# Optimization experiments

Hardware: AMD Instinct MI355X
Metric: run time of the kernel (lower is better)

Reference implementation:

```python
import jax, jax.numpy as jnp
import numpy as np

D_MODEL, N_HEADS, D_FF = 1024, 16, 4096
D_K = D_MODEL // N_HEADS
EPS = 1e-5


def setup_inputs() -> dict:
    key = jax.random.key(0)
    ks = jax.random.split(key, 16)
    s = 0.02
    p = {
        'x': jax.random.normal(ks[0], (2, 2048, D_MODEL), jnp.float32),
        'Wq': jax.random.normal(ks[1], (D_MODEL, D_MODEL), jnp.float32) * s,
        'bq': jnp.zeros((D_MODEL,), jnp.float32),
        'Wk': jax.random.normal(ks[2], (D_MODEL, D_MODEL), jnp.float32) * s,
        'bk': jnp.zeros((D_MODEL,), jnp.float32),
        'Wv': jax.random.normal(ks[3], (D_MODEL, D_MODEL), jnp.float32) * s,
        'bv': jnp.zeros((D_MODEL,), jnp.float32),
        'Wo': jax.random.normal(ks[4], (D_MODEL, D_MODEL), jnp.float32) * s,
        'bo': jnp.zeros((D_MODEL,), jnp.float32),
        'g1': jnp.ones((D_MODEL,), jnp.float32),
        'b1': jnp.zeros((D_MODEL,), jnp.float32),
        'W1': jax.random.normal(ks[5], (D_MODEL, D_FF), jnp.float32) * s,
        'bf1': jnp.zeros((D_FF,), jnp.float32),
        'W2': jax.random.normal(ks[6], (D_FF, D_MODEL), jnp.float32) * s,
        'bf2': jnp.zeros((D_MODEL,), jnp.float32),
        'g2': jnp.ones((D_MODEL,), jnp.float32),
        'b2': jnp.zeros((D_MODEL,), jnp.float32),
    }
    return p


def _layernorm(x, g, b):
    mu = jnp.mean(x, axis=-1, keepdims=True)
    var = jnp.var(x, axis=-1, keepdims=True)
    return (x - mu) * jax.lax.rsqrt(var + EPS) * g + b


def reference(x, Wq, bq, Wk, bk, Wv, bv, Wo, bo, g1, b1, W1, bf1, W2, bf2, g2, b2):
    B, S, _ = x.shape
    # project and split heads -> [B, H, S, d_k]
    def heads(y):
        return y.reshape(B, S, N_HEADS, D_K).transpose(0, 2, 1, 3)
    Q = heads(x @ Wq + bq)
    K = heads(x @ Wk + bk)
    V = heads(x @ Wv + bv)
    scores = jnp.einsum('bhqd,bhkd->bhqk', Q, K) / np.sqrt(D_K).astype(np.float32)
    attn = jax.nn.softmax(scores, axis=-1)  # dropout = identity (eval)
    ctx = jnp.einsum('bhqk,bhkd->bhqd', attn, V)
    ctx = ctx.transpose(0, 2, 1, 3).reshape(B, S, D_MODEL)
    attn_out = ctx @ Wo + bo
    h = _layernorm(x + attn_out, g1, b1)
    ff = (jax.nn.gelu(h @ W1 + bf1, approximate=False)) @ W2 + bf2
    out = _layernorm(h + ff, g2, b2)
    return out, attn
```

## Files before the change

kernel.cpp:

```cpp
#include <hip/hip_runtime.h>
#include <stdint.h>

#define SEQ 2048
#define BATCH 2
#define NH 16
#define DKH 64
#define DM 1024
#define DFF 4096
#define MTOT (BATCH*SEQ)

typedef __attribute__((ext_vector_type(8))) short bf16x8;
typedef __attribute__((ext_vector_type(4))) float f32x4;
typedef unsigned short ushort_t;

__device__ __forceinline__ unsigned short f2bf(float f) {
  union { float f; unsigned u; } c; c.f = f;
  return (unsigned short)((c.u + 0x7fffu + ((c.u >> 16) & 1u)) >> 16);
}

__device__ __forceinline__ void gload_lds16(const void* g, void* l) {
  __builtin_amdgcn_global_load_lds((__attribute__((address_space(1))) unsigned int*)g,
                                   (__attribute__((address_space(3))) unsigned int*)l,
                                   16, 0, 0);
}


__global__ __launch_bounds__(256) void conv_bf16(const float* __restrict__ X,
                                                 unsigned short* __restrict__ O, int n) {
  const int i = blockIdx.x * 256 + threadIdx.x;
  const int idx = i * 4;
  if (idx >= n) return;
  const float4 f = *(const float4*)(X + idx);
  ushort4 u; u.x = f2bf(f.x); u.y = f2bf(f.y); u.z = f2bf(f.z); u.w = f2bf(f.w);
  *(ushort4*)(O + idx) = u;
}

__global__ __launch_bounds__(256) void trans_conv(const float* __restrict__ W,
                                                  unsigned short* __restrict__ Wt,
                                                  int K, int N) {
  __shared__ float t[32][33];
  const int n0 = blockIdx.x * 32, k0 = blockIdx.y * 32;
  const int tx = threadIdx.x & 31, ty = threadIdx.x >> 5;
#pragma unroll
  for (int i = 0; i < 4; ++i)
    t[ty + i * 8][tx] = W[(long)(k0 + ty + i * 8) * N + n0 + tx];
  __syncthreads();
#pragma unroll
  for (int i = 0; i < 4; ++i)
    Wt[(long)(n0 + ty + i * 8) * K + k0 + tx] = f2bf(t[tx][ty + i * 8]);
}

__global__ __launch_bounds__(256) void trans_v(const unsigned short* __restrict__ V,
                                               unsigned short* __restrict__ Vt) {
  __shared__ unsigned short t[32][33];
  const int z = blockIdx.z, b = z >> 4, h = z & 15;
  const int s0 = blockIdx.x * 32, d0 = blockIdx.y * 32;
  const int tx = threadIdx.x & 31, ty = threadIdx.x >> 5;
#pragma unroll
  for (int i = 0; i < 4; ++i)
    t[ty + i * 8][tx] = V[(long)(b * SEQ + s0 + ty + i * 8) * DM + h * DKH + d0 + tx];
  __syncthreads();
#pragma unroll
  for (int i = 0; i < 4; ++i)
    Vt[((long)z * DKH + d0 + ty + i * 8) * SEQ + s0 + tx] = t[tx][ty + i * 8];
}

template <int EPI>
__global__ __launch_bounds__(256) void gemm_bt(
    const unsigned short* __restrict__ A, const unsigned short* __restrict__ Bt,
    float* __restrict__ Cf, unsigned short* __restrict__ Cbf,
    const float* __restrict__ bias, const float* __restrict__ resid,
    int M, int N, int K, int lda, int ldb, int ldc) {
  __shared__ unsigned short ldsA[128 * 32];
  __shared__ unsigned short ldsB[128 * 32];

  const int tid = threadIdx.x;
  const int lane = tid & 63, wave = tid >> 6;
  const int quad = lane >> 4, l16 = lane & 15;
  const int wm = (wave >> 1) * 64, wn = (wave & 1) * 64;
  const long tileM = (long)blockIdx.x * 128;
  const long tileN = (long)blockIdx.y * 128;

  const int srow = tid >> 2;
  const int scol = (tid & 3) * 8;
  const unsigned short* aSrc = A + (tileM + srow) * lda + scol;
  const unsigned short* bSrc = Bt + (tileN + srow) * ldb + scol;
  unsigned short* aDst = &ldsA[tid * 8];
  unsigned short* bDst = &ldsB[tid * 8];
  const long aRow64 = 64L * lda, bRow64 = 64L * ldb;

  f32x4 acc[4][4];
#pragma unroll
  for (int i = 0; i < 4; ++i)
#pragma unroll
    for (int j = 0; j < 4; ++j)
#pragma unroll
      for (int r = 0; r < 4; ++r) acc[i][j][r] = 0.f;

  for (int k0 = 0; k0 < K; k0 += 32) {
    __syncthreads();
    gload_lds16(aSrc + k0, aDst);
    gload_lds16(aSrc + aRow64 + k0, aDst + 2048);
    gload_lds16(bSrc + k0, bDst);
    gload_lds16(bSrc + bRow64 + k0, bDst + 2048);
    __syncthreads();

    bf16x8 aF[4], bF[4];
#pragma unroll
    for (int i = 0; i < 4; ++i)
      aF[i] = *(const bf16x8*)&ldsA[(wm + i * 16 + l16) * 32 + quad * 8];
#pragma unroll
    for (int j = 0; j < 4; ++j)
      bF[j] = *(const bf16x8*)&ldsB[(wn + j * 16 + l16) * 32 + quad * 8];
#pragma unroll
    for (int i = 0; i < 4; ++i)
#pragma unroll
      for (int j = 0; j < 4; ++j)
        acc[i][j] = __builtin_amdgcn_mfma_f32_16x16x32_bf16(aF[i], bF[j], acc[i][j], 0, 0, 0);
  }

#pragma unroll
  for (int i = 0; i < 4; ++i) {
    const long mb = tileM + wm + i * 16 + quad * 4;
#pragma unroll
    for (int j = 0; j < 4; ++j) {
      const long n = tileN + wn + j * 16 + l16;
      const float bv = bias[n];
#pragma unroll
      for (int r = 0; r < 4; ++r) {
        const long m = mb + r;
        const long idx = m * ldc + n;
        const float v = acc[i][j][r];
        if (EPI == 0) {
          Cbf[idx] = f2bf(v + bv);
        } else if (EPI == 2) {
          Cf[idx] = v + bv + resid[idx];
        } else {
          const float tt = v + bv;
          Cbf[idx] = f2bf(0.5f * tt * (1.f + erff(tt * 0.70710678118654752f)));
        }
      }
    }
  }
}

__global__ __launch_bounds__(256) void attn_stats(const unsigned short* __restrict__ Qbf,
                                                  const unsigned short* __restrict__ Kbf,
                                                  float2* __restrict__ stats) {
  const int z = blockIdx.z, b = z >> 4, h = z & 15;
  const int m0 = blockIdx.x * 128;

  __shared__ unsigned short ldsQ[2 * 128 * 32];
  __shared__ unsigned short ldsK[2 * 128 * 32];
  __shared__ float2 sm[4][64];

  const int tid = threadIdx.x;
  const int lane = tid & 63, wave = tid >> 6;
  const int quad = lane >> 4, l16 = lane & 15;
  const int wm = (wave >> 1) * 64, wn = (wave & 1) * 64;

  const unsigned short* Qbase = Qbf + ((long)(b * SEQ + m0)) * DM + h * DKH;
#pragma unroll
  for (int it = 0; it < 4; ++it) {
    const int c = it * 256 + tid;
    const int slab = c >> 9, row = (c >> 2) & 127, q = c & 3;
    gload_lds16(Qbase + (long)row * DM + slab * 32 + q * 8, &ldsQ[c * 8]);
  }

  float rm[4][4], rl[4][4];
#pragma unroll
  for (int i = 0; i < 4; ++i)
#pragma unroll
    for (int r = 0; r < 4; ++r) { rm[i][r] = -1e30f; rl[i][r] = 0.f; }

  for (int n = 0; n < 16; ++n) {
    __syncthreads();
    const unsigned short* Kbase = Kbf + ((long)(b * SEQ + n * 128)) * DM + h * DKH;
#pragma unroll
    for (int it = 0; it < 4; ++it) {
      const int c = it * 256 + tid;
      const int slab = c >> 9, row = (c >> 2) & 127, q = c & 3;
      gload_lds16(Kbase + (long)row * DM + slab * 32 + q * 8, &ldsK[c * 8]);
    }
    __syncthreads();

    f32x4 acc[4][4];
#pragma unroll
    for (int i = 0; i < 4; ++i)
#pragma unroll
      for (int j = 0; j < 4; ++j)
#pragma unroll
        for (int r = 0; r < 4; ++r) acc[i][j][r] = 0.f;

#pragma unroll
    for (int s = 0; s < 2; ++s) {
      bf16x8 aF[4], bF[4];
#pragma unroll
      for (int i = 0; i < 4; ++i)
        aF[i] = *(const bf16x8*)&ldsQ[(s * 128 + wm + i * 16 + l16) * 32 + quad * 8];
#pragma unroll
      for (int j = 0; j < 4; ++j)
        bF[j] = *(const bf16x8*)&ldsK[(s * 128 + wn + j * 16 + l16) * 32 + quad * 8];
#pragma unroll
      for (int i = 0; i < 4; ++i)
#pragma unroll
        for (int j = 0; j < 4; ++j)
          acc[i][j] = __builtin_amdgcn_mfma_f32_16x16x32_bf16(aF[i], bF[j], acc[i][j], 0, 0, 0);
    }

#pragma unroll
    for (int i = 0; i < 4; ++i)
#pragma unroll
      for (int r = 0; r < 4; ++r) {
        float v0 = acc[i][0][r] * 0.125f, v1 = acc[i][1][r] * 0.125f;
        float v2 = acc[i][2][r] * 0.125f, v3 = acc[i][3][r] * 0.125f;
        float tm = fmaxf(fmaxf(v0, v1), fmaxf(v2, v3));
#pragma unroll
        for (int o = 1; o < 16; o <<= 1) tm = fmaxf(tm, __shfl_xor(tm, o));
        const float mnew = fmaxf(rm[i][r], tm);
        float s4 = __expf(v0 - mnew) + __expf(v1 - mnew) +
                   __expf(v2 - mnew) + __expf(v3 - mnew);
#pragma unroll
        for (int o = 1; o < 16; o <<= 1) s4 += __shfl_xor(s4, o);
        rl[i][r] = rl[i][r] * __expf(rm[i][r] - mnew) + s4;
        rm[i][r] = mnew;
      }
  }

  if (l16 == 0) {
#pragma unroll
    for (int i = 0; i < 4; ++i)
#pragma unroll
      for (int r = 0; r < 4; ++r)
        sm[wave][i * 16 + quad * 4 + r] = make_float2(rm[i][r], rl[i][r]);
  }
  __syncthreads();
  if (tid < 128) {
    const int row = tid, g = row >> 6;
    const float2 a = sm[g * 2 + 0][row & 63];
    const float2 bb = sm[g * 2 + 1][row & 63];
    const float M = fmaxf(a.x, bb.x);
    const float Z = a.y * __expf(a.x - M) + bb.y * __expf(bb.x - M);
    stats[(long)z * SEQ + m0 + row] = make_float2(M, 1.f / Z);
  }
}

__global__ __launch_bounds__(256) void attn_fused(const unsigned short* __restrict__ Qbf,
                                                  const unsigned short* __restrict__ Kbf,
                                                  const unsigned short* __restrict__ Vt,
                                                  const float2* __restrict__ stats,
                                                  float* __restrict__ attn,
                                                  unsigned short* __restrict__ Ctx) {
  const int z = blockIdx.z, b = z >> 4, h = z & 15;
  const int m0 = blockIdx.x * 128;

  __shared__ unsigned short ldsQ[2 * 128 * 32];
  __shared__ unsigned short ldsK[2 * 128 * 32];
  __shared__ unsigned short ldsV[4 * 64 * 32];
  __shared__ unsigned short ldsP[4 * 128 * 32];

  const int tid = threadIdx.x;
  const int lane = tid & 63, wave = tid >> 6;
  const int quad = lane >> 4, l16 = lane & 15;
  const int wm = (wave >> 1) * 64, wn = (wave & 1) * 64;
  const int wm2 = (wave >> 1) * 64, wn2 = (wave & 1) * 32;

  const unsigned short* Qbase = Qbf + ((long)(b * SEQ + m0)) * DM + h * DKH;
#pragma unroll
  for (int it = 0; it < 4; ++it) {
    const int c = it * 256 + tid;
    const int slab = c >> 9, row = (c >> 2) & 127, q = c & 3;
    gload_lds16(Qbase + (long)row * DM + slab * 32 + q * 8, &ldsQ[c * 8]);
  }

  float sM[4][4], sI[4][4];
#pragma unroll
  for (int i = 0; i < 4; ++i)
#pragma unroll
    for (int r = 0; r < 4; ++r) {
      const float2 st = stats[(long)z * SEQ + m0 + wm + i * 16 + quad * 4 + r];
      sM[i][r] = st.x; sI[i][r] = st.y;
    }

  f32x4 acc_o[4][2];
#pragma unroll
  for (int i = 0; i < 4; ++i)
#pragma unroll
    for (int j = 0; j < 2; ++j)
#pragma unroll
      for (int r = 0; r < 4; ++r) acc_o[i][j][r] = 0.f;

  for (int n = 0; n < 16; ++n) {
    __syncthreads();
    const unsigned short* Kbase = Kbf + ((long)(b * SEQ + n * 128)) * DM + h * DKH;
#pragma unroll
    for (int it = 0; it < 4; ++it) {
      const int c = it * 256 + tid;
      const int slab = c >> 9, row = (c >> 2) & 127, q = c & 3;
      gload_lds16(Kbase + (long)row * DM + slab * 32 + q * 8, &ldsK[c * 8]);
    }
    const unsigned short* Vbase = Vt + (long)z * DKH * SEQ + n * 128;
#pragma unroll
    for (int it = 0; it < 4; ++it) {
      const int c = it * 256 + tid;
      const int slab = c >> 8, row = (c >> 2) & 63, q = c & 3;
      gload_lds16(Vbase + (long)row * SEQ + slab * 32 + q * 8, &ldsV[c * 8]);
    }
    __syncthreads();

    f32x4 acc[4][4];
#pragma unroll
    for (int i = 0; i < 4; ++i)
#pragma unroll
      for (int j = 0; j < 4; ++j)
#pragma unroll
        for (int r = 0; r < 4; ++r) acc[i][j][r] = 0.f;
#pragma unroll
    for (int s = 0; s < 2; ++s) {
      bf16x8 aF[4], bF[4];
#pragma unroll
      for (int i = 0; i < 4; ++i)
        aF[i] = *(const bf16x8*)&ldsQ[(s * 128 + wm + i * 16 + l16) * 32 + quad * 8];
#pragma unroll
      for (int j = 0; j < 4; ++j)
        bF[j] = *(const bf16x8*)&ldsK[(s * 128 + wn + j * 16 + l16) * 32 + quad * 8];
#pragma unroll
      for (int i = 0; i < 4; ++i)
#pragma unroll
        for (int j = 0; j < 4; ++j)
          acc[i][j] = __builtin_amdgcn_mfma_f32_16x16x32_bf16(aF[i], bF[j], acc[i][j], 0, 0, 0);
    }

    float* attnBase = attn + (long)z * SEQ * SEQ + (long)m0 * SEQ + n * 128;
#pragma unroll
    for (int i = 0; i < 4; ++i)
#pragma unroll
      for (int r = 0; r < 4; ++r) {
        const int rowl = wm + i * 16 + quad * 4 + r;
        const float M = sM[i][r], I = sI[i][r];
#pragma unroll
        for (int j = 0; j < 4; ++j) {
          const int col = wn + j * 16 + l16;
          const float p = __expf(acc[i][j][r] * 0.125f - M) * I;
          attnBase[(long)rowl * SEQ + col] = p;
          ldsP[((col >> 5) * 128 + rowl) * 32 + (col & 31)] = f2bf(p);
        }
      }
    __syncthreads();

#pragma unroll
    for (int slab = 0; slab < 4; ++slab) {
      bf16x8 aF[4], bF[2];
#pragma unroll
      for (int i = 0; i < 4; ++i)
        aF[i] = *(const bf16x8*)&ldsP[(slab * 128 + wm2 + i * 16 + l16) * 32 + quad * 8];
#pragma unroll
      for (int j = 0; j < 2; ++j)
        bF[j] = *(const bf16x8*)&ldsV[(slab * 64 + wn2 + j * 16 + l16) * 32 + quad * 8];
#pragma unroll
      for (int i = 0; i < 4; ++i)
#pragma unroll
        for (int j = 0; j < 2; ++j)
          acc_o[i][j] = __builtin_amdgcn_mfma_f32_16x16x32_bf16(aF[i], bF[j], acc_o[i][j], 0, 0, 0);
    }
  }

#pragma unroll
  for (int i = 0; i < 4; ++i)
#pragma unroll
    for (int j = 0; j < 2; ++j) {
      const int d = h * DKH + wn2 + j * 16 + l16;
#pragma unroll
      for (int r = 0; r < 4; ++r) {
        const long m = (long)b * SEQ + m0 + wm2 + i * 16 + quad * 4 + r;
        Ctx[m * DM + d] = f2bf(acc_o[i][j][r]);
      }
    }
}

__global__ __launch_bounds__(256) void layernorm_row(const float* __restrict__ Y,
                                                     const float* __restrict__ g,
                                                     const float* __restrict__ bb,
                                                     float* __restrict__ outF,
                                                     unsigned short* __restrict__ outBf) {
  const long row = blockIdx.x;
  const float* p = Y + row * DM;
  const int tid = threadIdx.x;
  const float4 v = *(const float4*)(p + tid * 4);
  float s = v.x + v.y + v.z + v.w;
  float ss = v.x * v.x + v.y * v.y + v.z * v.z + v.w * v.w;
#pragma unroll
  for (int o = 32; o > 0; o >>= 1) { s += __shfl_xor(s, o); ss += __shfl_xor(ss, o); }
  __shared__ float rs[4], rss[4];
  if ((tid & 63) == 0) { rs[tid >> 6] = s; rss[tid >> 6] = ss; }
  __syncthreads();
  s = rs[0] + rs[1] + rs[2] + rs[3];
  ss = rss[0] + rss[1] + rss[2] + rss[3];
  const float mu = s * (1.f / DM);
  const float var = ss * (1.f / DM) - mu * mu;
  const float rstd = rsqrtf(var + 1e-5f);
  const float4 gv = *(const float4*)(g + tid * 4);
  const float4 bv = *(const float4*)(bb + tid * 4);
  float4 o;
  o.x = (v.x - mu) * rstd * gv.x + bv.x;
  o.y = (v.y - mu) * rstd * gv.y + bv.y;
  o.z = (v.z - mu) * rstd * gv.z + bv.z;
  o.w = (v.w - mu) * rstd * gv.w + bv.w;
  *(float4*)(outF + row * DM + tid * 4) = o;
  if (outBf) {
    ushort4 u; u.x = f2bf(o.x); u.y = f2bf(o.y); u.z = f2bf(o.z); u.w = f2bf(o.w);
    *(ushort4*)(outBf + row * DM + tid * 4) = u;
  }
}

extern "C" void kernel_launch(void* const* d_in, const int* in_sizes, int n_in,
                              void* d_out, int out_size, void* d_ws, size_t ws_size,
                              hipStream_t stream) {
  (void)in_sizes; (void)n_in; (void)out_size; (void)ws_size;
  const float* x  = (const float*)d_in[0];
  const float* Wq = (const float*)d_in[1];
  const float* bq = (const float*)d_in[2];
  const float* Wk = (const float*)d_in[3];
  const float* bk = (const float*)d_in[4];
  const float* Wv = (const float*)d_in[5];
  const float* bv = (const float*)d_in[6];
  const float* Wo = (const float*)d_in[7];
  const float* bo = (const float*)d_in[8];
  const float* g1 = (const float*)d_in[9];
  const float* b1 = (const float*)d_in[10];
  const float* W1 = (const float*)d_in[11];
  const float* bf1 = (const float*)d_in[12];
  const float* W2 = (const float*)d_in[13];
  const float* bf2 = (const float*)d_in[14];
  const float* g2 = (const float*)d_in[15];
  const float* b2 = (const float*)d_in[16];

  float* out  = (float*)d_out;
  float* attn = out + (long)MTOT * DM;

  char* w = (char*)d_ws;
  const long MB = 1024L * 1024L;
  unsigned short* Wqt = (unsigned short*)(w + 0 * MB);
  unsigned short* Wkt = (unsigned short*)(w + 2 * MB);
  unsigned short* Wvt = (unsigned short*)(w + 4 * MB);
  unsigned short* Wot = (unsigned short*)(w + 6 * MB);
  unsigned short* W1t = (unsigned short*)(w + 8 * MB);
  unsigned short* W2t = (unsigned short*)(w + 16 * MB);
  unsigned short* xbf = (unsigned short*)(w + 24 * MB);
  unsigned short* hbf = xbf;
  unsigned short* Qbf = (unsigned short*)(w + 32 * MB);
  unsigned short* Kbf = (unsigned short*)(w + 40 * MB);
  unsigned short* Vt  = (unsigned short*)(w + 48 * MB);
  unsigned short* Vbf = (unsigned short*)(w + 56 * MB);
  unsigned short* ctxbf = Vbf;
  unsigned short* ffbf  = Qbf;
  float* y = (float*)(w + 64 * MB);
  float2* stats = (float2*)(w + 64 * MB);
  float* h = (float*)(w + 80 * MB);

  const dim3 blk(256);

  conv_bf16<<<dim3(MTOT * DM / 1024), blk, 0, stream>>>(x, xbf, MTOT * DM);
  trans_conv<<<dim3(DM / 32, DM / 32), blk, 0, stream>>>(Wq, Wqt, DM, DM);
  trans_conv<<<dim3(DM / 32, DM / 32), blk, 0, stream>>>(Wk, Wkt, DM, DM);
  trans_conv<<<dim3(DM / 32, DM / 32), blk, 0, stream>>>(Wv, Wvt, DM, DM);
  trans_conv<<<dim3(DM / 32, DM / 32), blk, 0, stream>>>(Wo, Wot, DM, DM);
  trans_conv<<<dim3(DFF / 32, DM / 32), blk, 0, stream>>>(W1, W1t, DM, DFF);
  trans_conv<<<dim3(DM / 32, DFF / 32), blk, 0, stream>>>(W2, W2t, DFF, DM);

  gemm_bt<0><<<dim3(MTOT / 128, DM / 128), blk, 0, stream>>>(
      xbf, Wqt, nullptr, Qbf, bq, nullptr, MTOT, DM, DM, DM, DM, DM);
  gemm_bt<0><<<dim3(MTOT / 128, DM / 128), blk, 0, stream>>>(
      xbf, Wkt, nullptr, Kbf, bk, nullptr, MTOT, DM, DM, DM, DM, DM);
  gemm_bt<0><<<dim3(MTOT / 128, DM / 128), blk, 0, stream>>>(
      xbf, Wvt, nullptr, Vbf, bv, nullptr, MTOT, DM, DM, DM, DM, DM);
  trans_v<<<dim3(SEQ / 32, DKH / 32, BATCH * NH), blk, 0, stream>>>(Vbf, Vt);

  attn_stats<<<dim3(SEQ / 128, 1, BATCH * NH), blk, 0, stream>>>(Qbf, Kbf, stats);
  attn_fused<<<dim3(SEQ / 128, 1, BATCH * NH), blk, 0, stream>>>(Qbf, Kbf, Vt, stats,
                                                                 attn, ctxbf);

  gemm_bt<2><<<dim3(MTOT / 128, DM / 128), blk, 0, stream>>>(
      ctxbf, Wot, y, nullptr, bo, x, MTOT, DM, DM, DM, DM, DM);
  layernorm_row<<<dim3(MTOT), blk, 0, stream>>>(y, g1, b1, h, hbf);

  gemm_bt<3><<<dim3(MTOT / 128, DFF / 128), blk, 0, stream>>>(
      hbf, W1t, nullptr, ffbf, bf1, nullptr, MTOT, DFF, DM, DM, DM, DFF);
  gemm_bt<2><<<dim3(MTOT / 128, DM / 128), blk, 0, stream>>>(
      ffbf, W2t, y, nullptr, bf2, h, MTOT, DM, DFF, DFF, DFF, DM);
  layernorm_row<<<dim3(MTOT), blk, 0, stream>>>(y, g2, b2, out, nullptr);
}
```

Measured before the change: 1.095 ms.

## Fuse QKV GEMM with V-transpose, merge attention passes, add split-K GEMMs

```diff
diff --git a/kernel.cpp b/kernel.cpp
--- a/kernel.cpp
+++ b/kernel.cpp
@@ -11,7 +11,6 @@
 
 typedef __attribute__((ext_vector_type(8))) short bf16x8;
 typedef __attribute__((ext_vector_type(4))) float f32x4;
-typedef unsigned short ushort_t;
 
 __device__ __forceinline__ unsigned short f2bf(float f) {
   union { float f; unsigned u; } c; c.f = f;
@@ -50,139 +49,301 @@
     Wt[(long)(n0 + ty + i * 8) * K + k0 + tx] = f2bf(t[tx][ty + i * 8]);
 }
 
-__global__ __launch_bounds__(256) void trans_v(const unsigned short* __restrict__ V,
-                                               unsigned short* __restrict__ Vt) {
-  __shared__ unsigned short t[32][33];
-  const int z = blockIdx.z, b = z >> 4, h = z & 15;
-  const int s0 = blockIdx.x * 32, d0 = blockIdx.y * 32;
-  const int tx = threadIdx.x & 31, ty = threadIdx.x >> 5;
-#pragma unroll
-  for (int i = 0; i < 4; ++i)
-    t[ty + i * 8][tx] = V[(long)(b * SEQ + s0 + ty + i * 8) * DM + h * DKH + d0 + tx];
-  __syncthreads();
-#pragma unroll
-  for (int i = 0; i < 4; ++i)
-    Vt[((long)z * DKH + d0 + ty + i * 8) * SEQ + s0 + tx] = t[tx][ty + i * 8];
-}
-
-template <int EPI>
-__global__ __launch_bounds__(256) void gemm_bt(
+__global__ __launch_bounds__(256) void concat3(const float* __restrict__ a,
+                                               const float* __restrict__ b,
+                                               const float* __restrict__ c,
+                                               float* __restrict__ o) {
+  const int i = blockIdx.x * 256 + threadIdx.x;
+  o[i] = i < 1024 ? a[i] : (i < 2048 ? b[i - 1024] : c[i - 2048]);
+}
+
+template <int EPI, int KS>
+__global__ __launch_bounds__(256 * KS) void gemm_bt(
     const unsigned short* __restrict__ A, const unsigned short* __restrict__ Bt,
     float* __restrict__ Cf, unsigned short* __restrict__ Cbf,
     const float* __restrict__ bias, const float* __restrict__ resid,
+    unsigned short* __restrict__ Vt,
     int M, int N, int K, int lda, int ldb, int ldc) {
-  __shared__ unsigned short ldsA[128 * 32];
-  __shared__ unsigned short ldsB[128 * 32];
+  (void)M; (void)N;
+  __shared__ unsigned short ldsAB[KS * 2 * 128 * 64];
+
+  const int tid = threadIdx.x;
+  const int ws = tid >> 8;
+  const int t2 = tid & 255;
+  const int lane = tid & 63;
+  const int w4 = (tid >> 6) & 3;
+  const int quad = lane >> 4, l16 = lane & 15;
+  const int wm = (w4 >> 1) * 64, wn = (w4 & 1) * 64;
+  const long tileM = (long)blockIdx.x * 128;
+  const long tileN = (long)blockIdx.y * 128;
+
+  unsigned short* ldsA = ldsAB + ws * 16384;
+  unsigned short* ldsB = ldsA + 8192;
+  const int kLen = K / KS;
+  const int kBase = ws * kLen;
+
+  const unsigned short* aS[4];
+  const unsigned short* bS[4];
+  int dOff[4];
+#pragma unroll
+  for (int it = 0; it < 4; ++it) {
+    const int c = it * 256 + t2;
+    const int slab = c >> 9, row = (c >> 2) & 127, q = c & 3;
+    aS[it] = A  + (tileM + row) * (long)lda + kBase + slab * 32 + q * 8;
+    bS[it] = Bt + (tileN + row) * (long)ldb + kBase + slab * 32 + q * 8;
+    dOff[it] = c * 8;
+  }
+
+  f32x4 acc[4][4];
+#pragma unroll
+  for (int i = 0; i < 4; ++i)
+#pragma unroll
+    for (int j = 0; j < 4; ++j)
+#pragma unroll
+      for (int r = 0; r < 4; ++r) acc[i][j][r] = 0.f;
+
+  for (int k0 = 0; k0 < kLen; k0 += 64) {
+    __syncthreads();
+#pragma unroll
+    for (int it = 0; it < 4; ++it) {
+      gload_lds16(aS[it] + k0, ldsA + dOff[it]);
+      gload_lds16(bS[it] + k0, ldsB + dOff[it]);
+    }
+    __syncthreads();
+#pragma unroll
+    for (int s = 0; s < 2; ++s) {
+      bf16x8 aF[4], bF[4];
+#pragma unroll
+      for (int i = 0; i < 4; ++i)
+        aF[i] = *(const bf16x8*)&ldsA[(s * 128 + wm + i * 16 + l16) * 32 + quad * 8];
+#pragma unroll
+      for (int j = 0; j < 4; ++j)
+        bF[j] = *(const bf16x8*)&ldsB[(s * 128 + wn + j * 16 + l16) * 32 + quad * 8];
+#pragma unroll
+      for (int i = 0; i < 4; ++i)
+#pragma unroll
+        for (int j = 0; j < 4; ++j)
+          acc[i][j] = __builtin_amdgcn_mfma_f32_16x16x32_bf16(aF[i], bF[j], acc[i][j], 0, 0, 0);
+    }
+  }
+
+  if constexpr (KS == 2) {
+    __syncthreads();
+    float* ldsF = (float*)ldsAB;
+    if (ws == 1) {
+#pragma unroll
+      for (int i = 0; i < 4; ++i)
+#pragma unroll
+        for (int j = 0; j < 4; ++j)
+#pragma unroll
+          for (int r = 0; r < 4; ++r)
+            ldsF[(wm + i * 16 + quad * 4 + r) * 128 + wn + j * 16 + l16] = acc[i][j][r];
+    }
+    __syncthreads();
+    if (ws == 1) return;
+#pragma unroll
+    for (int i = 0; i < 4; ++i)
+#pragma unroll
+      for (int j = 0; j < 4; ++j)
+#pragma unroll
+        for (int r = 0; r < 4; ++r)
+          acc[i][j][r] += ldsF[(wm + i * 16 + quad * 4 + r) * 128 + wn + j * 16 + l16];
+  }
+
+#pragma unroll
+  for (int i = 0; i < 4; ++i) {
+    const long mb = tileM + wm + i * 16 + quad * 4;
+#pragma unroll
+    for (int j = 0; j < 4; ++j) {
+      const long n = tileN + wn + j * 16 + l16;
+      const float bv = bias[n];
+      if (EPI == 4) {
+        if (n < 2048) {
+          unsigned short* dst = Cbf + (n >> 10) * ((long)MTOT * DM);
+          const int col = (int)n & 1023;
+#pragma unroll
+          for (int r = 0; r < 4; ++r)
+            dst[(mb + r) * DM + col] = f2bf(acc[i][j][r] + bv);
+        } else {
+          const int nn = (int)n - 2048;
+          const int bb2 = (int)(mb >> 11), s = (int)(mb & 2047);
+          const int zz = bb2 * 16 + (nn >> 6);
+          ushort4 u;
+          u.x = f2bf(acc[i][j][0] + bv); u.y = f2bf(acc[i][j][1] + bv);
+          u.z = f2bf(acc[i][j][2] + bv); u.w = f2bf(acc[i][j][3] + bv);
+          *(ushort4*)&Vt[((long)zz * DKH + (nn & 63)) * SEQ + s] = u;
+        }
+      } else {
+#pragma unroll
+        for (int r = 0; r < 4; ++r) {
+          const long m = mb + r;
+          const long idx = m * ldc + n;
+          const float v = acc[i][j][r];
+          if (EPI == 0) {
+            Cbf[idx] = f2bf(v + bv);
+          } else if (EPI == 2) {
+            Cf[idx] = v + bv + resid[idx];
+          } else {
+            const float tt = v + bv;
+            Cbf[idx] = f2bf(0.5f * tt * (1.f + erff(tt * 0.70710678118654752f)));
+          }
+        }
+      }
+    }
+  }
+}
+
+__device__ __forceinline__ void stage_k128(const unsigned short* __restrict__ gbase,
+                                           unsigned short* lds, int tid) {
+#pragma unroll
+  for (int it = 0; it < 4; ++it) {
+    const int c = it * 256 + tid;
+    const int slab = c >> 9, row = (c >> 2) & 127, q = c & 3;
+    gload_lds16(gbase + (long)row * DM + slab * 32 + q * 8, lds + c * 8);
+  }
+}
+__device__ __forceinline__ void stage_v64(const unsigned short* __restrict__ gbase,
+                                          unsigned short* lds, int tid) {
+#pragma unroll
+  for (int it = 0; it < 4; ++it) {
+    const int c = it * 256 + tid;
+    const int slab = c >> 8, row = (c >> 2) & 63, q = c & 3;
+    gload_lds16(gbase + (long)row * SEQ + slab * 32 + q * 8, lds + c * 8);
+  }
+}
+
+__global__ __launch_bounds__(256) void attn_all(const unsigned short* __restrict__ Qbf,
+                                                const unsigned short* __restrict__ Kbf,
+                                                const unsigned short* __restrict__ Vt,
+                                                float* __restrict__ attn,
+                                                unsigned short* __restrict__ Ctx) {
+  const int z = blockIdx.z, b = z >> 4, h = z & 15;
+  const int m0 = blockIdx.x * 128;
+
+  __shared__ unsigned short ldsQ[2 * 128 * 32];
+  __shared__ unsigned short ldsK[2 * 128 * 32];
+  __shared__ unsigned short ldsV[4 * 64 * 32];
+  __shared__ unsigned short ldsP[4 * 128 * 32];
 
   const int tid = threadIdx.x;
   const int lane = tid & 63, wave = tid >> 6;
   const int quad = lane >> 4, l16 = lane & 15;
   const int wm = (wave >> 1) * 64, wn = (wave & 1) * 64;
-  const long tileM = (long)blockIdx.x * 128;
-  const long tileN = (long)blockIdx.y * 128;
-
-  const int srow = tid >> 2;
-  const int scol = (tid & 3) * 8;
-  const unsigned short* aSrc = A + (tileM + srow) * lda + scol;
-  const unsigned short* bSrc = Bt + (tileN + srow) * ldb + scol;
-  unsigned short* aDst = &ldsA[tid * 8];
-  unsigned short* bDst = &ldsB[tid * 8];
-  const long aRow64 = 64L * lda, bRow64 = 64L * ldb;
-
-  f32x4 acc[4][4];
-#pragma unroll
-  for (int i = 0; i < 4; ++i)
-#pragma unroll
-    for (int j = 0; j < 4; ++j)
-#pragma unroll
-      for (int r = 0; r < 4; ++r) acc[i][j][r] = 0.f;
-
-  for (int k0 = 0; k0 < K; k0 += 32) {
-    __syncthreads();
-    gload_lds16(aSrc + k0, aDst);
-    gload_lds16(aSrc + aRow64 + k0, aDst + 2048);
-    gload_lds16(bSrc + k0, bDst);
-    gload_lds16(bSrc + bRow64 + k0, bDst + 2048);
-    __syncthreads();
-
-    bf16x8 aF[4], bF[4];
-#pragma unroll
-    for (int i = 0; i < 4; ++i)
-      aF[i] = *(const bf16x8*)&ldsA[(wm + i * 16 + l16) * 32 + quad * 8];
-#pragma unroll
-    for (int j = 0; j < 4; ++j)
-      bF[j] = *(const bf16x8*)&ldsB[(wn + j * 16 + l16) * 32 + quad * 8];
+  const int wn2 = (wave & 1) * 32;
+
+  const unsigned short* Qbase = Qbf + ((long)(b * SEQ + m0)) * DM + h * DKH;
+  const unsigned short* Kz = Kbf + ((long)b * SEQ) * DM + h * DKH;
+  const unsigned short* Vz = Vt + (long)z * DKH * SEQ;
+
+  stage_k128(Qbase, ldsQ, tid);
+  stage_k128(Kz, ldsK, tid);
+  __syncthreads();
+
+  bf16x8 qF[2][4];
+#pragma unroll
+  for (int s = 0; s < 2; ++s)
+#pragma unroll
+    for (int i = 0; i < 4; ++i)
+      qF[s][i] = *(const bf16x8*)&ldsQ[(s * 128 + wm + i * 16 + l16) * 32 + quad * 8];
+  __syncthreads();
+
+  float rm[4][4], rl[4][4];
+#pragma unroll
+  for (int i = 0; i < 4; ++i)
+#pragma unroll
+    for (int r = 0; r < 4; ++r) { rm[i][r] = -1e30f; rl[i][r] = 0.f; }
+
+  for (int n = 0; n < 16; ++n) {
+    if (n) __syncthreads();
+    if (n < 15) stage_k128(Kz + (long)(n + 1) * 128 * DM, (n & 1) ? ldsK : ldsQ, tid);
+    const unsigned short* kc = (n & 1) ? ldsQ : ldsK;
+
+    f32x4 acc[4][4];
 #pragma unroll
     for (int i = 0; i < 4; ++i)
 #pragma unroll
       for (int j = 0; j < 4; ++j)
-        acc[i][j] = __builtin_amdgcn_mfma_f32_16x16x32_bf16(aF[i], bF[j], acc[i][j], 0, 0, 0);
-  }
-
-#pragma unroll
-  for (int i = 0; i < 4; ++i) {
-    const long mb = tileM + wm + i * 16 + quad * 4;
-#pragma unroll
-    for (int j = 0; j < 4; ++j) {
-      const long n = tileN + wn + j * 16 + l16;
-      const float bv = bias[n];
+#pragma unroll
+        for (int r = 0; r < 4; ++r) acc[i][j][r] = 0.f;
+#pragma unroll
+    for (int s = 0; s < 2; ++s) {
+      bf16x8 bF[4];
+#pragma unroll
+      for (int j = 0; j < 4; ++j)
+        bF[j] = *(const bf16x8*)&kc[(s * 128 + wn + j * 16 + l16) * 32 + quad * 8];
+#pragma unroll
+      for (int i = 0; i < 4; ++i)
+#pragma unroll
+        for (int j = 0; j < 4; ++j)
+          acc[i][j] = __builtin_amdgcn_mfma_f32_16x16x32_bf16(qF[s][i], bF[j], acc[i][j], 0, 0, 0);
+    }
+#pragma unroll
+    for (int i = 0; i < 4; ++i)
 #pragma unroll
       for (int r = 0; r < 4; ++r) {
-        const long m = mb + r;
-        const long idx = m * ldc + n;
-        const float v = acc[i][j][r];
-        if (EPI == 0) {
-          Cbf[idx] = f2bf(v + bv);
-        } else if (EPI == 2) {
-          Cf[idx] = v + bv + resid[idx];
-        } else {
-          const float tt = v + bv;
-          Cbf[idx] = f2bf(0.5f * tt * (1.f + erff(tt * 0.70710678118654752f)));
-        }
+        const float v0 = acc[i][0][r] * 0.125f, v1 = acc[i][1][r] * 0.125f;
+        const float v2 = acc[i][2][r] * 0.125f, v3 = acc[i][3][r] * 0.125f;
+        const float tm = fmaxf(fmaxf(v0, v1), fmaxf(v2, v3));
+        const float mn = fmaxf(rm[i][r], tm);
+        rl[i][r] = rl[i][r] * __expf(rm[i][r] - mn) +
+                   __expf(v0 - mn) + __expf(v1 - mn) + __expf(v2 - mn) + __expf(v3 - mn);
+        rm[i][r] = mn;
       }
-    }
-  }
-}
-
-__global__ __launch_bounds__(256) void attn_stats(const unsigned short* __restrict__ Qbf,
-                                                  const unsigned short* __restrict__ Kbf,
-                                                  float2* __restrict__ stats) {
-  const int z = blockIdx.z, b = z >> 4, h = z & 15;
-  const int m0 = blockIdx.x * 128;
-
-  __shared__ unsigned short ldsQ[2 * 128 * 32];
-  __shared__ unsigned short ldsK[2 * 128 * 32];
-  __shared__ float2 sm[4][64];
-
-  const int tid = threadIdx.x;
-  const int lane = tid & 63, wave = tid >> 6;
-  const int quad = lane >> 4, l16 = lane & 15;
-  const int wm = (wave >> 1) * 64, wn = (wave & 1) * 64;
-
-  const unsigned short* Qbase = Qbf + ((long)(b * SEQ + m0)) * DM + h * DKH;
-#pragma unroll
-  for (int it = 0; it < 4; ++it) {
-    const int c = it * 256 + tid;
-    const int slab = c >> 9, row = (c >> 2) & 127, q = c & 3;
-    gload_lds16(Qbase + (long)row * DM + slab * 32 + q * 8, &ldsQ[c * 8]);
-  }
-
-  float rm[4][4], rl[4][4];
-#pragma unroll
-  for (int i = 0; i < 4; ++i)
-#pragma unroll
-    for (int r = 0; r < 4; ++r) { rm[i][r] = -1e30f; rl[i][r] = 0.f; }
+  }
+
+#pragma unroll
+  for (int i = 0; i < 4; ++i)
+#pragma unroll
+    for (int r = 0; r < 4; ++r) {
+      float m = rm[i][r], l = rl[i][r];
+#pragma unroll
+      for (int o = 1; o < 16; o <<= 1) {
+        const float om = __shfl_xor(m, o), ol = __shfl_xor(l, o);
+        const float mn = fmaxf(m, om);
+        l = l * __expf(m - mn) + ol * __expf(om - mn);
+        m = mn;
+      }
+      rm[i][r] = m; rl[i][r] = l;
+    }
+
+  float2* sm = (float2*)ldsP;
+  if (l16 == 0) {
+#pragma unroll
+    for (int i = 0; i < 4; ++i)
+#pragma unroll
+      for (int r = 0; r < 4; ++r)
+        sm[wave * 64 + i * 16 + quad * 4 + r] = make_float2(rm[i][r], rl[i][r]);
+  }
+  __syncthreads();
+  float sM[4][4], sI[4][4];
+#pragma unroll
+  for (int i = 0; i < 4; ++i)
+#pragma unroll
+    for (int r = 0; r < 4; ++r) {
+      const int rr = i * 16 + quad * 4 + r;
+      const float2 A = sm[(wave & ~1) * 64 + rr];
+      const float2 B = sm[((wave & ~1) + 1) * 64 + rr];
+      const float M = fmaxf(A.x, B.x);
+      const float Z = A.y * __expf(A.x - M) + B.y * __expf(B.x - M);
+      sM[i][r] = M; sI[i][r] = 1.f / Z;
+    }
+
+  f32x4 acc_o[4][2];
+#pragma unroll
+  for (int i = 0; i < 4; ++i)
+#pragma unroll
+    for (int j = 0; j < 2; ++j)
+#pragma unroll
+      for (int r = 0; r < 4; ++r) acc_o[i][j][r] = 0.f;
+
+  stage_k128(Kz, ldsK, tid);
+  __syncthreads();
 
   for (int n = 0; n < 16; ++n) {
-    __syncthreads();
-    const unsigned short* Kbase = Kbf + ((long)(b * SEQ + n * 128)) * DM + h * DKH;
-#pragma unroll
-    for (int it = 0; it < 4; ++it) {
-      const int c = it * 256 + tid;
-      const int slab = c >> 9, row = (c >> 2) & 127, q = c & 3;
-      gload_lds16(Kbase + (long)row * DM + slab * 32 + q * 8, &ldsK[c * 8]);
-    }
-    __syncthreads();
+    if (n) __syncthreads();
+    if (n < 15) stage_k128(Kz + (long)(n + 1) * 128 * DM, (n & 1) ? ldsK : ldsQ, tid);
+    stage_v64(Vz + n * 128, ldsV, tid);
+    const unsigned short* kc = (n & 1) ? ldsQ : ldsK;
 
     f32x4 acc[4][4];
 #pragma unroll
@@ -191,145 +352,20 @@
       for (int j = 0; j < 4; ++j)
 #pragma unroll
         for (int r = 0; r < 4; ++r) acc[i][j][r] = 0.f;
-
+    __builtin_amdgcn_s_setprio(1);
 #pragma unroll
     for (int s = 0; s < 2; ++s) {
-      bf16x8 aF[4], bF[4];
-#pragma unroll
-      for (int i = 0; i < 4; ++i)
-        aF[i] = *(const bf16x8*)&ldsQ[(s * 128 + wm + i * 16 + l16) * 32 + quad * 8];
+      bf16x8 bF[4];
 #pragma unroll
       for (int j = 0; j < 4; ++j)
-        bF[j] = *(const bf16x8*)&ldsK[(s * 128 + wn + j * 16 + l16) * 32 + quad * 8];
+        bF[j] = *(const bf16x8*)&kc[(s * 128 + wn + j * 16 + l16) * 32 + quad * 8];
 #pragma unroll
       for (int i = 0; i < 4; ++i)
 #pragma unroll
         for (int j = 0; j < 4; ++j)
-          acc[i][j] = __builtin_amdgcn_mfma_f32_16x16x32_bf16(aF[i], bF[j], acc[i][j], 0, 0, 0);
-    }
-
-#pragma unroll
-    for (int i = 0; i < 4; ++i)
-#pragma unroll
-      for (int r = 0; r < 4; ++r) {
-        float v0 = acc[i][0][r] * 0.125f, v1 = acc[i][1][r] * 0.125f;
-        float v2 = acc[i][2][r] * 0.125f, v3 = acc[i][3][r] * 0.125f;
-        float tm = fmaxf(fmaxf(v0, v1), fmaxf(v2, v3));
-#pragma unroll
-        for (int o = 1; o < 16; o <<= 1) tm = fmaxf(tm, __shfl_xor(tm, o));
-        const float mnew = fmaxf(rm[i][r], tm);
-        float s4 = __expf(v0 - mnew) + __expf(v1 - mnew) +
-                   __expf(v2 - mnew) + __expf(v3 - mnew);
-#pragma unroll
-        for (int o = 1; o < 16; o <<= 1) s4 += __shfl_xor(s4, o);
-        rl[i][r] = rl[i][r] * __expf(rm[i][r] - mnew) + s4;
-        rm[i][r] = mnew;
-      }
-  }
-
-  if (l16 == 0) {
-#pragma unroll
-    for (int i = 0; i < 4; ++i)
-#pragma unroll
-      for (int r = 0; r < 4; ++r)
-        sm[wave][i * 16 + quad * 4 + r] = make_float2(rm[i][r], rl[i][r]);
-  }
-  __syncthreads();
-  if (tid < 128) {
-    const int row = tid, g = row >> 6;
-    const float2 a = sm[g * 2 + 0][row & 63];
-    const float2 bb = sm[g * 2 + 1][row & 63];
-    const float M = fmaxf(a.x, bb.x);
-    const float Z = a.y * __expf(a.x - M) + bb.y * __expf(bb.x - M);
-    stats[(long)z * SEQ + m0 + row] = make_float2(M, 1.f / Z);
-  }
-}
-
-__global__ __launch_bounds__(256) void attn_fused(const unsigned short* __restrict__ Qbf,
-                                                  const unsigned short* __restrict__ Kbf,
-                                                  const unsigned short* __restrict__ Vt,
-                                                  const float2* __restrict__ stats,
-                                                  float* __restrict__ attn,
-                                                  unsigned short* __restrict__ Ctx) {
-  const int z = blockIdx.z, b = z >> 4, h = z & 15;
-  const int m0 = blockIdx.x * 128;
-
-  __shared__ unsigned short ldsQ[2 * 128 * 32];
-  __shared__ unsigned short ldsK[2 * 128 * 32];
-  __shared__ unsigned short ldsV[4 * 64 * 32];
-  __shared__ unsigned short ldsP[4 * 128 * 32];
-
-  const int tid = threadIdx.x;
-  const int lane = tid & 63, wave = tid >> 6;
-  const int quad = lane >> 4, l16 = lane & 15;
-  const int wm = (wave >> 1) * 64, wn = (wave & 1) * 64;
-  const int wm2 = (wave >> 1) * 64, wn2 = (wave & 1) * 32;
-
-  const unsigned short* Qbase = Qbf + ((long)(b * SEQ + m0)) * DM + h * DKH;
-#pragma unroll
-  for (int it = 0; it < 4; ++it) {
-    const int c = it * 256 + tid;
-    const int slab = c >> 9, row = (c >> 2) & 127, q = c & 3;
-    gload_lds16(Qbase + (long)row * DM + slab * 32 + q * 8, &ldsQ[c * 8]);
-  }
-
-  float sM[4][4], sI[4][4];
-#pragma unroll
-  for (int i = 0; i < 4; ++i)
-#pragma unroll
-    for (int r = 0; r < 4; ++r) {
-      const float2 st = stats[(long)z * SEQ + m0 + wm + i * 16 + quad * 4 + r];
-      sM[i][r] = st.x; sI[i][r] = st.y;
-    }
-
-  f32x4 acc_o[4][2];
-#pragma unroll
-  for (int i = 0; i < 4; ++i)
-#pragma unroll
-    for (int j = 0; j < 2; ++j)
-#pragma unroll
-      for (int r = 0; r < 4; ++r) acc_o[i][j][r] = 0.f;
-
-  for (int n = 0; n < 16; ++n) {
-    __syncthreads();
-    const unsigned short* Kbase = Kbf + ((long)(b * SEQ + n * 128)) * DM + h * DKH;
-#pragma unroll
-    for (int it = 0; it < 4; ++it) {
-      const int c = it * 256 + tid;
-      const int slab = c >> 9, row = (c >> 2) & 127, q = c & 3;
-      gload_lds16(Kbase + (long)row * DM + slab * 32 + q * 8, &ldsK[c * 8]);
-    }
-    const unsigned short* Vbase = Vt + (long)z * DKH * SEQ + n * 128;
-#pragma unroll
-    for (int it = 0; it < 4; ++it) {
-      const int c = it * 256 + tid;
-      const int slab = c >> 8, row = (c >> 2) & 63, q = c & 3;
-      gload_lds16(Vbase + (long)row * SEQ + slab * 32 + q * 8, &ldsV[c * 8]);
-    }
-    __syncthreads();
-
-    f32x4 acc[4][4];
-#pragma unroll
-    for (int i = 0; i < 4; ++i)
-#pragma unroll
-      for (int j = 0; j < 4; ++j)
-#pragma unroll
-        for (int r = 0; r < 4; ++r) acc[i][j][r] = 0.f;
-#pragma unroll
-    for (int s = 0; s < 2; ++s) {
-      bf16x8 aF[4], bF[4];
-#pragma unroll
-      for (int i = 0; i < 4; ++i)
-        aF[i] = *(const bf16x8*)&ldsQ[(s * 128 + wm + i * 16 + l16) * 32 + quad * 8];
-#pragma unroll
-      for (int j = 0; j < 4; ++j)
-        bF[j] = *(const bf16x8*)&ldsK[(s * 128 + wn + j * 16 + l16) * 32 + quad * 8];
-#pragma unroll
-      for (int i = 0; i < 4; ++i)
-#pragma unroll
-        for (int j = 0; j < 4; ++j)
-          acc[i][j] = __builtin_amdgcn_mfma_f32_16x16x32_bf16(aF[i], bF[j], acc[i][j], 0, 0, 0);
-    }
+          acc[i][j] = __builtin_amdgcn_mfma_f32_16x16x32_bf16(qF[s][i], bF[j], acc[i][j], 0, 0, 0);
+    }
+    __builtin_amdgcn_s_setprio(0);
 
     float* attnBase = attn + (long)z * SEQ * SEQ + (long)m0 * SEQ + n * 128;
 #pragma unroll
@@ -348,12 +384,13 @@
       }
     __syncthreads();
 
+    __builtin_amdgcn_s_setprio(1);
 #pragma unroll
     for (int slab = 0; slab < 4; ++slab) {
       bf16x8 aF[4], bF[2];
 #pragma unroll
       for (int i = 0; i < 4; ++i)
-        aF[i] = *(const bf16x8*)&ldsP[(slab * 128 + wm2 + i * 16 + l16) * 32 + quad * 8];
+        aF[i] = *(const bf16x8*)&ldsP[(slab * 128 + wm + i * 16 + l16) * 32 + quad * 8];
 #pragma unroll
       for (int j = 0; j < 2; ++j)
         bF[j] = *(const bf16x8*)&ldsV[(slab * 64 + wn2 + j * 16 + l16) * 32 + quad * 8];
@@ -363,6 +400,7 @@
         for (int j = 0; j < 2; ++j)
           acc_o[i][j] = __builtin_amdgcn_mfma_f32_16x16x32_bf16(aF[i], bF[j], acc_o[i][j], 0, 0, 0);
     }
+    __builtin_amdgcn_s_setprio(0);
   }
 
 #pragma unroll
@@ -372,7 +410,7 @@
       const int d = h * DKH + wn2 + j * 16 + l16;
 #pragma unroll
       for (int r = 0; r < 4; ++r) {
-        const long m = (long)b * SEQ + m0 + wm2 + i * 16 + quad * 4 + r;
+        const long m = (long)b * SEQ + m0 + wm + i * 16 + quad * 4 + r;
         Ctx[m * DM + d] = f2bf(acc_o[i][j][r]);
       }
     }
@@ -440,53 +478,44 @@
 
   char* w = (char*)d_ws;
   const long MB = 1024L * 1024L;
-  unsigned short* Wqt = (unsigned short*)(w + 0 * MB);
-  unsigned short* Wkt = (unsigned short*)(w + 2 * MB);
-  unsigned short* Wvt = (unsigned short*)(w + 4 * MB);
-  unsigned short* Wot = (unsigned short*)(w + 6 * MB);
-  unsigned short* W1t = (unsigned short*)(w + 8 * MB);
-  unsigned short* W2t = (unsigned short*)(w + 16 * MB);
-  unsigned short* xbf = (unsigned short*)(w + 24 * MB);
-  unsigned short* hbf = xbf;
-  unsigned short* Qbf = (unsigned short*)(w + 32 * MB);
-  unsigned short* Kbf = (unsigned short*)(w + 40 * MB);
-  unsigned short* Vt  = (unsigned short*)(w + 48 * MB);
-  unsigned short* Vbf = (unsigned short*)(w + 56 * MB);
-  unsigned short* ctxbf = Vbf;
+  unsigned short* Wqkvt = (unsigned short*)(w + 0 * MB);
+  unsigned short* Wot   = (unsigned short*)(w + 6 * MB);
+  unsigned short* W1t   = (unsigned short*)(w + 8 * MB);
+  unsigned short* W2t   = (unsigned short*)(w + 16 * MB);
+  unsigned short* xbf   = (unsigned short*)(w + 24 * MB);
+  unsigned short* hbf   = xbf;
+  unsigned short* Qbf   = (unsigned short*)(w + 32 * MB);
+  unsigned short* Kbf   = (unsigned short*)(w + 40 * MB);
+  unsigned short* Vt    = (unsigned short*)(w + 48 * MB);
+  unsigned short* ctxbf = (unsigned short*)(w + 56 * MB);
   unsigned short* ffbf  = Qbf;
-  float* y = (float*)(w + 64 * MB);
-  float2* stats = (float2*)(w + 64 * MB);
-  float* h = (float*)(w + 80 * MB);
-
-  const dim3 blk(256);
+  float* bqkv = (float*)(w + 64 * MB);
+  float* y    = (float*)(w + 64 * MB);
+  float* h    = (float*)(w + 80 * MB);
+
+  const dim3 blk(256), blk2(512);
 
   conv_bf16<<<dim3(MTOT * DM / 1024), blk, 0, stream>>>(x, xbf, MTOT * DM);
-  trans_conv<<<dim3(DM / 32, DM / 32), blk, 0, stream>>>(Wq, Wqt, DM, DM);
-  trans_conv<<<dim3(DM / 32, DM / 32), blk, 0, stream>>>(Wk, Wkt, DM, DM);
-  trans_conv<<<dim3(DM / 32, DM / 32), blk, 0, stream>>>(Wv, Wvt, DM, DM);
+  trans_conv<<<dim3(DM / 32, DM / 32), blk, 0, stream>>>(Wq, Wqkvt, DM, DM);
+  trans_conv<<<dim3(DM / 32, DM / 32), blk, 0, stream>>>(Wk, Wqkvt + 1024 * 1024, DM, DM);
+  trans_conv<<<dim3(DM / 32, DM / 32), blk, 0, stream>>>(Wv, Wqkvt + 2 * 1024 * 1024, DM, DM);
   trans_conv<<<dim3(DM / 32, DM / 32), blk, 0, stream>>>(Wo, Wot, DM, DM);
   trans_conv<<<dim3(DFF / 32, DM / 32), blk, 0, stream>>>(W1, W1t, DM, DFF);
   trans_conv<<<dim3(DM / 32, DFF / 32), blk, 0, stream>>>(W2, W2t, DFF, DM);
-
-  gemm_bt<0><<<dim3(MTOT / 128, DM / 128), blk, 0, stream>>>(
-      xbf, Wqt, nullptr, Qbf, bq, nullptr, MTOT, DM, DM, DM, DM, DM);
-  gemm_bt<0><<<dim3(MTOT / 128, DM / 128), blk, 0, stream>>>(
-      xbf, Wkt, nullptr, Kbf, bk, nullptr, MTOT, DM, DM, DM, DM, DM);
-  gemm_bt<0><<<dim3(MTOT / 128, DM / 128), blk, 0, stream>>>(
-      xbf, Wvt, nullptr, Vbf, bv, nullptr, MTOT, DM, DM, DM, DM, DM);
-  trans_v<<<dim3(SEQ / 32, DKH / 32, BATCH * NH), blk, 0, stream>>>(Vbf, Vt);
-
-  attn_stats<<<dim3(SEQ / 128, 1, BATCH * NH), blk, 0, stream>>>(Qbf, Kbf, stats);
-  attn_fused<<<dim3(SEQ / 128, 1, BATCH * NH), blk, 0, stream>>>(Qbf, Kbf, Vt, stats,
-                                                                 attn, ctxbf);
-
-  gemm_bt<2><<<dim3(MTOT / 128, DM / 128), blk, 0, stream>>>(
-      ctxbf, Wot, y, nullptr, bo, x, MTOT, DM, DM, DM, DM, DM);
+  concat3<<<dim3(12), blk, 0, stream>>>(bq, bk, bv, bqkv);
+
+  gemm_bt<4, 1><<<dim3(MTOT / 128, 3072 / 128), blk, 0, stream>>>(
+      xbf, Wqkvt, nullptr, Qbf, bqkv, nullptr, Vt, MTOT, 3072, DM, DM, DM, DM);
+
+  attn_all<<<dim3(SEQ / 128, 1, BATCH * NH), blk, 0, stream>>>(Qbf, Kbf, Vt, attn, ctxbf);
+
+  gemm_bt<2, 2><<<dim3(MTOT / 128, DM / 128), blk2, 0, stream>>>(
+      ctxbf, Wot, y, nullptr, bo, x, nullptr, MTOT, DM, DM, DM, DM, DM);
   layernorm_row<<<dim3(MTOT), blk, 0, stream>>>(y, g1, b1, h, hbf);
 
-  gemm_bt<3><<<dim3(MTOT / 128, DFF / 128), blk, 0, stream>>>(
-      hbf, W1t, nullptr, ffbf, bf1, nullptr, MTOT, DFF, DM, DM, DM, DFF);
-  gemm_bt<2><<<dim3(MTOT / 128, DM / 128), blk, 0, stream>>>(
-      ffbf, W2t, y, nullptr, bf2, h, MTOT, DM, DFF, DFF, DFF, DM);
+  gemm_bt<3, 1><<<dim3(MTOT / 128, DFF / 128), blk, 0, stream>>>(
+      hbf, W1t, nullptr, ffbf, bf1, nullptr, nullptr, MTOT, DFF, DM, DM, DM, DFF);
+  gemm_bt<2, 2><<<dim3(MTOT / 128, DM / 128), blk2, 0, stream>>>(
+      ffbf, W2t, y, nullptr, bf2, h, nullptr, MTOT, DM, DFF, DFF, DFF, DM);
   layernorm_row<<<dim3(MTOT), blk, 0, stream>>>(y, g2, b2, out, nullptr);
 }
```

Measured after the change: 970.5 us. 11.4% less time.
